# Kernel tuning notes

Measured on AMD Instinct MI355X. Metric: run time of the kernel, lower is better.

## Reference

```python
import jax, jax.numpy as jnp
import numpy as np

N = 50000
E = 800000
D_IN, D_HID, D_OUT = 256, 512, 256
LN_EPS = 1e-5


def setup_inputs() -> dict:
    key = jax.random.key(0)
    ks = jax.random.split(key, 8)
    return {
        "v": jax.random.normal(ks[0], (N, D_IN), dtype=jnp.float32),
        "edge_weight": jax.random.uniform(ks[1], (E,), dtype=jnp.float32),
        "epsilon": jnp.zeros((1, 1), dtype=jnp.float32),
        "w1": jax.random.normal(ks[2], (D_HID, D_IN), dtype=jnp.float32) * (1.0 / np.sqrt(D_IN)),
        "b1": jnp.zeros((D_HID,), dtype=jnp.float32),
        "g1": jnp.ones((D_HID,), dtype=jnp.float32),
        "beta1": jnp.zeros((D_HID,), dtype=jnp.float32),
        "w2": jax.random.normal(ks[3], (D_OUT, D_HID), dtype=jnp.float32) * (1.0 / np.sqrt(D_HID)),
        "b2": jnp.zeros((D_OUT,), dtype=jnp.float32),
        "g2": jnp.ones((D_OUT,), dtype=jnp.float32),
        "beta2": jnp.zeros((D_OUT,), dtype=jnp.float32),
        "src": jax.random.randint(ks[4], (E,), 0, N, dtype=jnp.int32),
        "dst": jax.random.randint(ks[5], (E,), 0, N, dtype=jnp.int32),
    }


def _layer_norm(x, g, b):
    mu = jnp.mean(x, axis=-1, keepdims=True)
    var = jnp.mean(jnp.square(x - mu), axis=-1, keepdims=True)
    return (x - mu) * jax.lax.rsqrt(var + LN_EPS) * g + b


def reference(v, edge_weight, epsilon, w1, b1, g1, beta1, w2, b2, g2, beta2, src, dst):
    # sparse adjacency aggregation: agg[dst] += w * v[src]   (torch.sparse.mm(a, v))
    msgs = v[src] * edge_weight[:, None]            # [E, D_IN]
    agg = jax.ops.segment_sum(msgs, dst, num_segments=v.shape[0])  # [N, D_IN]
    h = agg + epsilon * v                            # epsilon residual
    # MLP: Linear -> LayerNorm -> ReLU  (x2)
    h = jax.nn.relu(_layer_norm(h @ w1.T + b1, g1, beta1))
    h = jax.nn.relu(_layer_norm(h @ w2.T + b2, g2, beta2))
    return h
```

## Files before the change

kernel.cpp:

```cpp
#include <hip/hip_runtime.h>

#define D_IN 256
#define D_HID 512
#define D_OUT 256
#define LN_EPS 1e-5f
#define SCAN_B 512

typedef __attribute__((ext_vector_type(8))) short bf16x8;
typedef __attribute__((ext_vector_type(4))) float f32x4;

__device__ __forceinline__ ushort f2bf(float x) {
    union { float f; unsigned u; } c; c.f = x;
    unsigned r = c.u + 0x7FFFu + ((c.u >> 16) & 1u);
    return (ushort)(r >> 16);
}
__device__ __forceinline__ float bf2f(unsigned b) {
    union { unsigned u; float f; } c; c.u = b << 16;
    return c.f;
}

__global__ void prep_kernel(const float* __restrict__ v, const float* __restrict__ w1,
                            const float* __restrict__ w2, ushort* __restrict__ vb,
                            ushort* __restrict__ w1p, ushort* __restrict__ w2p,
                            int* __restrict__ cnt, int n4v, int nzero,
                            int bv, int bw) {
    int b = blockIdx.x, t = threadIdx.x;
    if (b < bv) {
        int i = b * 256 + t;
        if (i < n4v) {
            float4 x = ((const float4*)v)[i];
            ((ushort4*)vb)[i] = make_ushort4(f2bf(x.x), f2bf(x.y), f2bf(x.z), f2bf(x.w));
        }
    } else if (b < bv + bw) {
        int j = (b - bv) * 256 + t;
        if (j < 32768) {
            int f = j * 4;
            int row = f >> 8, col = f & 255;
            float4 x = ((const float4*)w1)[j];
            int rb = row >> 4, fr = row & 15;
            int kb32 = col >> 5, q = (col & 31) >> 3, e = col & 7;
            int chunk = (kb32 * 32 + rb) * 64 + q * 16 + fr;
            *(ushort4*)(w1p + chunk * 8 + e) =
                make_ushort4(f2bf(x.x), f2bf(x.y), f2bf(x.z), f2bf(x.w));
        } else {
            int k = j - 32768;
            int f = k * 4;
            int row = f >> 9, col = f & 511;
            float4 x = ((const float4*)w2)[k];
            int rb = row >> 4, fr = row & 15;
            int kb32 = col >> 5, q = (col & 31) >> 3, e = col & 7;
            int chunk = (kb32 * 16 + rb) * 64 + q * 16 + fr;
            *(ushort4*)(w2p + chunk * 8 + e) =
                make_ushort4(f2bf(x.x), f2bf(x.y), f2bf(x.z), f2bf(x.w));
        }
    } else {
        int i = (b - bv - bw) * 256 + t;
        if (i < nzero) cnt[i] = 0;
    }
}

__global__ void hist_kernel(const int* __restrict__ dst, int* __restrict__ cnt, int E) {
    int e = blockIdx.x * 256 + threadIdx.x;
    if (e < E) atomicAdd(&cnt[dst[e]], 1);
}

__global__ __launch_bounds__(SCAN_B) void scan1_kernel(const int* __restrict__ cnt,
                                                       int* __restrict__ offs,
                                                       int* __restrict__ bsum, int n) {
    __shared__ int s[SCAN_B];
    int i = blockIdx.x * SCAN_B + threadIdx.x;
    int x = (i < n) ? cnt[i] : 0;
    s[threadIdx.x] = x;
    __syncthreads();
    for (int o = 1; o < SCAN_B; o <<= 1) {
        int t = (threadIdx.x >= (unsigned)o) ? s[threadIdx.x - o] : 0;
        __syncthreads();
        s[threadIdx.x] += t;
        __syncthreads();
    }
    if (i < n) offs[i] = s[threadIdx.x] - x;
    if (threadIdx.x == SCAN_B - 1) bsum[blockIdx.x] = s[threadIdx.x];
}

__global__ __launch_bounds__(SCAN_B) void scan3_kernel(int* __restrict__ offs,
                                                       int* __restrict__ cursor,
                                                       const int* __restrict__ bsum,
                                                       int n, int E, int nb) {
    __shared__ int s[SCAN_B];
    int t = threadIdx.x;
    s[t] = (t < nb && t < (int)blockIdx.x) ? bsum[t] : 0;
    __syncthreads();
    for (int o = SCAN_B / 2; o > 0; o >>= 1) {
        if (t < o) s[t] += s[t + o];
        __syncthreads();
    }
    int base = s[0];
    int i = blockIdx.x * SCAN_B + t;
    if (i < n) {
        int v0 = offs[i] + base;
        offs[i] = v0;
        cursor[i] = v0;
    }
    if (i == 0) offs[n] = E;
}

__global__ void fill_kernel(const int* __restrict__ src, const int* __restrict__ dst,
                            const float* __restrict__ ew, int* __restrict__ cursor,
                            int2* __restrict__ perm, int E) {
    int e = blockIdx.x * 256 + threadIdx.x;
    if (e >= E) return;
    int p = atomicAdd(&cursor[dst[e]], 1);
    perm[p] = make_int2(src[e], __float_as_int(ew[e]));
}

__global__ __launch_bounds__(256) void aggregate_kernel(
    const ushort* __restrict__ vb, const float* __restrict__ eps_p,
    const int* __restrict__ offs, const int2* __restrict__ perm,
    ushort* __restrict__ aggb, int N) {
    int node = blockIdx.x * 4 + (threadIdx.x >> 6);
    if (node >= N) return;
    int lane = threadIdx.x & 63;
    int beg = offs[node], end = offs[node + 1];
    float a0 = 0.f, a1 = 0.f, a2 = 0.f, a3 = 0.f;
    float c0 = 0.f, c1 = 0.f, c2 = 0.f, c3 = 0.f;

    int i = beg;
    for (; i + 8 <= end; i += 8) {
        int2 p0 = perm[i + 0], p1 = perm[i + 1], p2 = perm[i + 2], p3 = perm[i + 3];
        int2 p4 = perm[i + 4], p5 = perm[i + 5], p6 = perm[i + 6], p7 = perm[i + 7];
        float w0 = __int_as_float(p0.y), w1 = __int_as_float(p1.y);
        float w2 = __int_as_float(p2.y), w3 = __int_as_float(p3.y);
        float w4 = __int_as_float(p4.y), w5 = __int_as_float(p5.y);
        float w6 = __int_as_float(p6.y), w7 = __int_as_float(p7.y);
        ushort4 r0 = ((const ushort4*)(vb + (size_t)p0.x * D_IN))[lane];
        ushort4 r1 = ((const ushort4*)(vb + (size_t)p1.x * D_IN))[lane];
        ushort4 r2 = ((const ushort4*)(vb + (size_t)p2.x * D_IN))[lane];
        ushort4 r3 = ((const ushort4*)(vb + (size_t)p3.x * D_IN))[lane];
        ushort4 r4 = ((const ushort4*)(vb + (size_t)p4.x * D_IN))[lane];
        ushort4 r5 = ((const ushort4*)(vb + (size_t)p5.x * D_IN))[lane];
        ushort4 r6 = ((const ushort4*)(vb + (size_t)p6.x * D_IN))[lane];
        ushort4 r7 = ((const ushort4*)(vb + (size_t)p7.x * D_IN))[lane];
        a0 += w0 * bf2f(r0.x) + w1 * bf2f(r1.x) + w2 * bf2f(r2.x) + w3 * bf2f(r3.x);
        a1 += w0 * bf2f(r0.y) + w1 * bf2f(r1.y) + w2 * bf2f(r2.y) + w3 * bf2f(r3.y);
        a2 += w0 * bf2f(r0.z) + w1 * bf2f(r1.z) + w2 * bf2f(r2.z) + w3 * bf2f(r3.z);
        a3 += w0 * bf2f(r0.w) + w1 * bf2f(r1.w) + w2 * bf2f(r2.w) + w3 * bf2f(r3.w);
        c0 += w4 * bf2f(r4.x) + w5 * bf2f(r5.x) + w6 * bf2f(r6.x) + w7 * bf2f(r7.x);
        c1 += w4 * bf2f(r4.y) + w5 * bf2f(r5.y) + w6 * bf2f(r6.y) + w7 * bf2f(r7.y);
        c2 += w4 * bf2f(r4.z) + w5 * bf2f(r5.z) + w6 * bf2f(r6.z) + w7 * bf2f(r7.z);
        c3 += w4 * bf2f(r4.w) + w5 * bf2f(r5.w) + w6 * bf2f(r6.w) + w7 * bf2f(r7.w);
    }
    for (; i + 4 <= end; i += 4) {
        int2 p0 = perm[i + 0], p1 = perm[i + 1], p2 = perm[i + 2], p3 = perm[i + 3];
        float w0 = __int_as_float(p0.y), w1 = __int_as_float(p1.y);
        float w2 = __int_as_float(p2.y), w3 = __int_as_float(p3.y);
        ushort4 r0 = ((const ushort4*)(vb + (size_t)p0.x * D_IN))[lane];
        ushort4 r1 = ((const ushort4*)(vb + (size_t)p1.x * D_IN))[lane];
        ushort4 r2 = ((const ushort4*)(vb + (size_t)p2.x * D_IN))[lane];
        ushort4 r3 = ((const ushort4*)(vb + (size_t)p3.x * D_IN))[lane];
        a0 += w0 * bf2f(r0.x) + w1 * bf2f(r1.x) + w2 * bf2f(r2.x) + w3 * bf2f(r3.x);
        a1 += w0 * bf2f(r0.y) + w1 * bf2f(r1.y) + w2 * bf2f(r2.y) + w3 * bf2f(r3.y);
        a2 += w0 * bf2f(r0.z) + w1 * bf2f(r1.z) + w2 * bf2f(r2.z) + w3 * bf2f(r3.z);
        a3 += w0 * bf2f(r0.w) + w1 * bf2f(r1.w) + w2 * bf2f(r2.w) + w3 * bf2f(r3.w);
    }
    for (; i < end; ++i) {
        int2 p = perm[i];
        float w = __int_as_float(p.y);
        ushort4 r = ((const ushort4*)(vb + (size_t)p.x * D_IN))[lane];
        a0 += w * bf2f(r.x); a1 += w * bf2f(r.y);
        a2 += w * bf2f(r.z); a3 += w * bf2f(r.w);
    }
    a0 += c0; a1 += c1; a2 += c2; a3 += c3;
    float eps = eps_p[0];
    ushort4 m = ((const ushort4*)(vb + (size_t)node * D_IN))[lane];
    a0 += eps * bf2f(m.x); a1 += eps * bf2f(m.y);
    a2 += eps * bf2f(m.z); a3 += eps * bf2f(m.w);
    ((ushort4*)(aggb + (size_t)node * D_IN))[lane] =
        make_ushort4(f2bf(a0), f2bf(a1), f2bf(a2), f2bf(a3));
}

#define HS_IDX(row, col) ((row) * 512 + ((col) ^ (((row) & 7) << 3)))
#define AT_IDX(row, col) ((row) * 256 + ((col) ^ (((row) & 7) << 3)))

__global__ __launch_bounds__(256, 2) void mlp_kernel(
    const ushort* __restrict__ A, const ushort* __restrict__ w1p,
    const ushort* __restrict__ w2p,
    const float* __restrict__ b1, const float* __restrict__ g1, const float* __restrict__ be1,
    const float* __restrict__ b2, const float* __restrict__ g2, const float* __restrict__ be2,
    float* __restrict__ out, int N) {
    __shared__ ushort hs[32768];
    __shared__ float redf[640];

    int t = threadIdx.x;
    int w = t >> 6, lane = t & 63;
    int row0 = blockIdx.x * 64;
    int fr = lane & 15, q = lane >> 4, kb = q * 8;

    #pragma unroll
    for (int j = 0; j < 8; ++j) {
        int p = (w * 8 + j) * 64 + lane;
        int row = p >> 5, cbs = p & 31;
        int colblk = cbs ^ (row & 7);
        int ar = row0 + row; if (ar > N - 1) ar = N - 1;
        const ushort* gp = A + (size_t)ar * D_IN + colblk * 8;
        __builtin_amdgcn_global_load_lds(
            (const __attribute__((address_space(1))) void*)gp,
            (__attribute__((address_space(3))) void*)(&hs[(w * 8 + j) * 512]),
            16, 0, 0);
    }

    bf16x8 bfb[2][8];
    #pragma unroll
    for (int c = 0; c < 8; ++c)
        bfb[0][c] = *(const bf16x8*)(w1p + (size_t)((0 * 32 + w * 8 + c) * 64 + lane) * 8);

    __syncthreads();

    f32x4 acc[4][8];
    #pragma unroll
    for (int m = 0; m < 4; ++m)
        #pragma unroll
        for (int c = 0; c < 8; ++c) {
            f32x4 z = {0.f, 0.f, 0.f, 0.f};
            acc[m][c] = z;
        }

    #pragma unroll
    for (int ks = 0; ks < 8; ++ks) {
        const int cur = ks & 1, nxt = cur ^ 1;
        if (ks < 7) {
            #pragma unroll
            for (int c = 0; c < 8; ++c)
                bfb[nxt][c] = *(const bf16x8*)(w1p +
                    (size_t)(((ks + 1) * 32 + w * 8 + c) * 64 + lane) * 8);
        }
        bf16x8 af[4];
        #pragma unroll
        for (int m = 0; m < 4; ++m)
            af[m] = *(const bf16x8*)&hs[AT_IDX(m * 16 + fr, ks * 32 + kb)];
        #pragma unroll
        for (int m = 0; m < 4; ++m)
            #pragma unroll
            for (int c = 0; c < 8; ++c)
                acc[m][c] = __builtin_amdgcn_mfma_f32_16x16x32_bf16(af[m], bfb[cur][c], acc[m][c], 0, 0, 0);
    }

    {
        float bi[8], gg[8], bb[8];
        #pragma unroll
        for (int c = 0; c < 8; ++c) {
            int col = w * 128 + c * 16 + fr;
            bi[c] = b1[col]; gg[c] = g1[col]; bb[c] = be1[col];
        }
        #pragma unroll
        for (int m = 0; m < 4; ++m) {
            #pragma unroll
            for (int r = 0; r < 4; ++r) {
                float s = 0.f, sq = 0.f;
                #pragma unroll
                for (int c = 0; c < 8; ++c) {
                    float x = acc[m][c][r] + bi[c];
                    acc[m][c][r] = x;
                    s += x; sq += x * x;
                }
                #pragma unroll
                for (int o = 1; o < 16; o <<= 1) {
                    s  += __shfl_xor(s, o, 64);
                    sq += __shfl_xor(sq, o, 64);
                }
                if (fr == 0) {
                    int row = m * 16 + q * 4 + r;
                    redf[row * 4 + w]       = s;
                    redf[256 + row * 4 + w] = sq;
                }
            }
        }
        __syncthreads();
        if (t < 64) {
            float s  = redf[t * 4 + 0] + redf[t * 4 + 1] + redf[t * 4 + 2] + redf[t * 4 + 3];
            float sq = redf[256 + t * 4 + 0] + redf[256 + t * 4 + 1] +
                       redf[256 + t * 4 + 2] + redf[256 + t * 4 + 3];
            float mu = s / (float)D_HID;
            float var = sq / (float)D_HID - mu * mu;
            redf[512 + t] = mu;
            redf[576 + t] = rsqrtf(var + LN_EPS);
        }
        __syncthreads();
        #pragma unroll
        for (int m = 0; m < 4; ++m) {
            #pragma unroll
            for (int r = 0; r < 4; ++r) {
                int row = m * 16 + q * 4 + r;
                float mu = redf[512 + row], rs = redf[576 + row];
                #pragma unroll
                for (int c = 0; c < 8; ++c) {
                    int col = w * 128 + c * 16 + fr;
                    float y = (acc[m][c][r] - mu) * rs * gg[c] + bb[c];
                    hs[HS_IDX(row, col)] = f2bf(fmaxf(y, 0.f));
                }
            }
        }
    }

    bf16x8 bf2b[2][4][2];
    #pragma unroll
    for (int c = 0; c < 4; ++c)
        #pragma unroll
        for (int h = 0; h < 2; ++h)
            bf2b[0][c][h] = *(const bf16x8*)(w2p +
                (size_t)(((0 + h) * 16 + w * 4 + c) * 64 + lane) * 8);

    __syncthreads();

    f32x4 acc2[4][4];
    #pragma unroll
    for (int m = 0; m < 4; ++m)
        #pragma unroll
        for (int c = 0; c < 4; ++c) {
            f32x4 z = {0.f, 0.f, 0.f, 0.f};
            acc2[m][c] = z;
        }

    #pragma unroll
    for (int s = 0; s < 8; ++s) {
        const int cur = s & 1, nxt = cur ^ 1;
        if (s < 7) {
            #pragma unroll
            for (int c = 0; c < 4; ++c)
                #pragma unroll
                for (int h = 0; h < 2; ++h)
                    bf2b[nxt][c][h] = *(const bf16x8*)(w2p +
                        (size_t)(((2 * (s + 1) + h) * 16 + w * 4 + c) * 64 + lane) * 8);
        }
        bf16x8 af2[4][2];
        #pragma unroll
        for (int m = 0; m < 4; ++m)
            #pragma unroll
            for (int h = 0; h < 2; ++h)
                af2[m][h] = *(const bf16x8*)&hs[HS_IDX(m * 16 + fr, s * 64 + h * 32 + kb)];
        #pragma unroll
        for (int m = 0; m < 4; ++m)
            #pragma unroll
            for (int c = 0; c < 4; ++c)
                #pragma unroll
                for (int h = 0; h < 2; ++h)
                    acc2[m][c] = __builtin_amdgcn_mfma_f32_16x16x32_bf16(af2[m][h], bf2b[cur][c][h], acc2[m][c], 0, 0, 0);
    }

    {
        float bi[4], gg[4], bb[4];
        #pragma unroll
        for (int c = 0; c < 4; ++c) {
            int col = w * 64 + c * 16 + fr;
            bi[c] = b2[col]; gg[c] = g2[col]; bb[c] = be2[col];
        }
        #pragma unroll
        for (int m = 0; m < 4; ++m) {
            #pragma unroll
            for (int r = 0; r < 4; ++r) {
                float s = 0.f, sq = 0.f;
                #pragma unroll
                for (int c = 0; c < 4; ++c) {
                    float x = acc2[m][c][r] + bi[c];
                    acc2[m][c][r] = x;
                    s += x; sq += x * x;
                }
                #pragma unroll
                for (int o = 1; o < 16; o <<= 1) {
                    s  += __shfl_xor(s, o, 64);
                    sq += __shfl_xor(sq, o, 64);
                }
                if (fr == 0) {
                    int row = m * 16 + q * 4 + r;
                    redf[row * 4 + w]       = s;
                    redf[256 + row * 4 + w] = sq;
                }
            }
        }
        __syncthreads();
        if (t < 64) {
            float s  = redf[t * 4 + 0] + redf[t * 4 + 1] + redf[t * 4 + 2] + redf[t * 4 + 3];
            float sq = redf[256 + t * 4 + 0] + redf[256 + t * 4 + 1] +
                       redf[256 + t * 4 + 2] + redf[256 + t * 4 + 3];
            float mu = s / (float)D_OUT;
            float var = sq / (float)D_OUT - mu * mu;
            redf[512 + t] = mu;
            redf[576 + t] = rsqrtf(var + LN_EPS);
        }
        __syncthreads();
        #pragma unroll
        for (int m = 0; m < 4; ++m) {
            #pragma unroll
            for (int r = 0; r < 4; ++r) {
                int row = m * 16 + q * 4 + r;
                int grow = row0 + row;
                if (grow >= N) continue;
                float mu = redf[512 + row], rs = redf[576 + row];
                #pragma unroll
                for (int c = 0; c < 4; ++c) {
                    int col = w * 64 + c * 16 + fr;
                    float y = (acc2[m][c][r] - mu) * rs * gg[c] + bb[c];
                    out[(size_t)grow * D_OUT + col] = fmaxf(y, 0.f);
                }
            }
        }
    }
}

extern "C" void kernel_launch(void* const* d_in, const int* in_sizes, int n_in,
                              void* d_out, int out_size, void* d_ws, size_t ws_size,
                              hipStream_t stream) {
    const float* v     = (const float*)d_in[0];
    const float* ew    = (const float*)d_in[1];
    const float* eps   = (const float*)d_in[2];
    const float* w1    = (const float*)d_in[3];
    const float* b1    = (const float*)d_in[4];
    const float* g1    = (const float*)d_in[5];
    const float* beta1 = (const float*)d_in[6];
    const float* w2    = (const float*)d_in[7];
    const float* b2    = (const float*)d_in[8];
    const float* g2    = (const float*)d_in[9];
    const float* beta2 = (const float*)d_in[10];
    const int*   src   = (const int*)d_in[11];
    const int*   dst   = (const int*)d_in[12];

    int N = in_sizes[0] / D_IN;
    int E = in_sizes[1];

    float* out = (float*)d_out;

    char* ws = (char*)d_ws;
    size_t off = 0;
    ushort* vb   = (ushort*)(ws + off); off += (size_t)N * D_IN * 2;
    ushort* aggb = (ushort*)(ws + off); off += (size_t)N * D_IN * 2;
    ushort* w1p  = (ushort*)(ws + off); off += (size_t)D_HID * D_IN * 2;
    ushort* w2p  = (ushort*)(ws + off); off += (size_t)D_OUT * D_HID * 2;
    int* offs     = (int*)(ws + off); off += (size_t)(N + 256) * 4;
    int* cursor   = (int*)(ws + off); off += (size_t)(N + 256) * 4;
    int* bsum     = (int*)(ws + off); off += 1024;
    int2* perm    = (int2*)(ws + off); off += (size_t)E * 8;

    int nb = (N + SCAN_B - 1) / SCAN_B;
    int n4v = N * (D_IN / 4);
    int bv = (n4v + 255) / 256;
    int bw = 256;
    int bz = (N + 255) / 256;

    prep_kernel<<<bv + bw + bz, 256, 0, stream>>>(v, w1, w2, vb, w1p, w2p,
                                                  cursor, n4v, N, bv, bw);

    hist_kernel<<<(E + 255) / 256, 256, 0, stream>>>(dst, cursor, E);
    scan1_kernel<<<nb, SCAN_B, 0, stream>>>(cursor, offs, bsum, N);
    scan3_kernel<<<nb, SCAN_B, 0, stream>>>(offs, cursor, bsum, N, E, nb);
    fill_kernel<<<(E + 255) / 256, 256, 0, stream>>>(src, dst, ew, cursor, perm, E);

    aggregate_kernel<<<(N + 3) / 4, 256, 0, stream>>>(vb, eps, offs, perm, aggb, N);

    int mblocks = (N + 63) / 64;
    mlp_kernel<<<mblocks, 256, 0, stream>>>(aggb, w1p, w2p,
                                            b1, g1, beta1, b2, g2, beta2, out, N);
}
```

Measured before the change: 322.6 us.

## Fuse aggregation into MLP kernel and build CSR with atomic ranks

Moves the gather-aggregation into the MLP kernel so each block aggregates its 64 rows straight into shared memory, which removes the aggb intermediate write/read and one kernel launch. The CSR build now records each edge's atomic rank during the histogram (merged into prep_kernel), so fill computes positions without a second atomic pass. Zeroing moves to hipMemsetAsync. The risk is that the MLP kernel now does the latency-bound gather with only 4 waves per block and 2 blocks per CU, so the aggregation may get less parallelism than the separate kernel had. It also adds an extra rank array write and read.

```diff
diff --git a/kernel.cpp b/kernel.cpp
--- a/kernel.cpp
+++ b/kernel.cpp
@@ -22,7 +22,8 @@
 __global__ void prep_kernel(const float* __restrict__ v, const float* __restrict__ w1,
                             const float* __restrict__ w2, ushort* __restrict__ vb,
                             ushort* __restrict__ w1p, ushort* __restrict__ w2p,
-                            int* __restrict__ cnt, int n4v, int nzero,
+                            const int* __restrict__ dst, int* __restrict__ rank,
+                            int* __restrict__ cnt, int n4v, int E,
                             int bv, int bw) {
     int b = blockIdx.x, t = threadIdx.x;
     if (b < bv) {
@@ -54,14 +55,9 @@
                 make_ushort4(f2bf(x.x), f2bf(x.y), f2bf(x.z), f2bf(x.w));
         }
     } else {
-        int i = (b - bv - bw) * 256 + t;
-        if (i < nzero) cnt[i] = 0;
-    }
-}
-
-__global__ void hist_kernel(const int* __restrict__ dst, int* __restrict__ cnt, int E) {
-    int e = blockIdx.x * 256 + threadIdx.x;
-    if (e < E) atomicAdd(&cnt[dst[e]], 1);
+        int e = (b - bv - bw) * 256 + t;
+        if (e < E) rank[e] = atomicAdd(&cnt[dst[e]], 1);
+    }
 }
 
 __global__ __launch_bounds__(SCAN_B) void scan1_kernel(const int* __restrict__ cnt,
@@ -83,7 +79,6 @@
 }
 
 __global__ __launch_bounds__(SCAN_B) void scan3_kernel(int* __restrict__ offs,
-                                                       int* __restrict__ cursor,
                                                        const int* __restrict__ bsum,
                                                        int n, int E, int nb) {
     __shared__ int s[SCAN_B];
@@ -96,94 +91,27 @@
     }
     int base = s[0];
     int i = blockIdx.x * SCAN_B + t;
-    if (i < n) {
-        int v0 = offs[i] + base;
-        offs[i] = v0;
-        cursor[i] = v0;
-    }
+    if (i < n) offs[i] += base;
     if (i == 0) offs[n] = E;
 }
 
 __global__ void fill_kernel(const int* __restrict__ src, const int* __restrict__ dst,
-                            const float* __restrict__ ew, int* __restrict__ cursor,
+                            const float* __restrict__ ew, const int* __restrict__ rank,
+                            const int* __restrict__ offs,
                             int2* __restrict__ perm, int E) {
     int e = blockIdx.x * 256 + threadIdx.x;
     if (e >= E) return;
-    int p = atomicAdd(&cursor[dst[e]], 1);
+    int p = offs[dst[e]] + rank[e];
     perm[p] = make_int2(src[e], __float_as_int(ew[e]));
 }
 
-__global__ __launch_bounds__(256) void aggregate_kernel(
+#define HS_IDX(row, col) ((row) * 512 + ((col) ^ (((row) & 7) << 3)))
+#define AT_IDX(row, col) ((row) * 256 + ((col) ^ (((row) & 7) << 3)))
+
+__global__ __launch_bounds__(256, 2) void mlp_kernel(
     const ushort* __restrict__ vb, const float* __restrict__ eps_p,
     const int* __restrict__ offs, const int2* __restrict__ perm,
-    ushort* __restrict__ aggb, int N) {
-    int node = blockIdx.x * 4 + (threadIdx.x >> 6);
-    if (node >= N) return;
-    int lane = threadIdx.x & 63;
-    int beg = offs[node], end = offs[node + 1];
-    float a0 = 0.f, a1 = 0.f, a2 = 0.f, a3 = 0.f;
-    float c0 = 0.f, c1 = 0.f, c2 = 0.f, c3 = 0.f;
-
-    int i = beg;
-    for (; i + 8 <= end; i += 8) {
-        int2 p0 = perm[i + 0], p1 = perm[i + 1], p2 = perm[i + 2], p3 = perm[i + 3];
-        int2 p4 = perm[i + 4], p5 = perm[i + 5], p6 = perm[i + 6], p7 = perm[i + 7];
-        float w0 = __int_as_float(p0.y), w1 = __int_as_float(p1.y);
-        float w2 = __int_as_float(p2.y), w3 = __int_as_float(p3.y);
-        float w4 = __int_as_float(p4.y), w5 = __int_as_float(p5.y);
-        float w6 = __int_as_float(p6.y), w7 = __int_as_float(p7.y);
-        ushort4 r0 = ((const ushort4*)(vb + (size_t)p0.x * D_IN))[lane];
-        ushort4 r1 = ((const ushort4*)(vb + (size_t)p1.x * D_IN))[lane];
-        ushort4 r2 = ((const ushort4*)(vb + (size_t)p2.x * D_IN))[lane];
-        ushort4 r3 = ((const ushort4*)(vb + (size_t)p3.x * D_IN))[lane];
-        ushort4 r4 = ((const ushort4*)(vb + (size_t)p4.x * D_IN))[lane];
-        ushort4 r5 = ((const ushort4*)(vb + (size_t)p5.x * D_IN))[lane];
-        ushort4 r6 = ((const ushort4*)(vb + (size_t)p6.x * D_IN))[lane];
-        ushort4 r7 = ((const ushort4*)(vb + (size_t)p7.x * D_IN))[lane];
-        a0 += w0 * bf2f(r0.x) + w1 * bf2f(r1.x) + w2 * bf2f(r2.x) + w3 * bf2f(r3.x);
-        a1 += w0 * bf2f(r0.y) + w1 * bf2f(r1.y) + w2 * bf2f(r2.y) + w3 * bf2f(r3.y);
-        a2 += w0 * bf2f(r0.z) + w1 * bf2f(r1.z) + w2 * bf2f(r2.z) + w3 * bf2f(r3.z);
-        a3 += w0 * bf2f(r0.w) + w1 * bf2f(r1.w) + w2 * bf2f(r2.w) + w3 * bf2f(r3.w);
-        c0 += w4 * bf2f(r4.x) + w5 * bf2f(r5.x) + w6 * bf2f(r6.x) + w7 * bf2f(r7.x);
-        c1 += w4 * bf2f(r4.y) + w5 * bf2f(r5.y) + w6 * bf2f(r6.y) + w7 * bf2f(r7.y);
-        c2 += w4 * bf2f(r4.z) + w5 * bf2f(r5.z) + w6 * bf2f(r6.z) + w7 * bf2f(r7.z);
-        c3 += w4 * bf2f(r4.w) + w5 * bf2f(r5.w) + w6 * bf2f(r6.w) + w7 * bf2f(r7.w);
-    }
-    for (; i + 4 <= end; i += 4) {
-        int2 p0 = perm[i + 0], p1 = perm[i + 1], p2 = perm[i + 2], p3 = perm[i + 3];
-        float w0 = __int_as_float(p0.y), w1 = __int_as_float(p1.y);
-        float w2 = __int_as_float(p2.y), w3 = __int_as_float(p3.y);
-        ushort4 r0 = ((const ushort4*)(vb + (size_t)p0.x * D_IN))[lane];
-        ushort4 r1 = ((const ushort4*)(vb + (size_t)p1.x * D_IN))[lane];
-        ushort4 r2 = ((const ushort4*)(vb + (size_t)p2.x * D_IN))[lane];
-        ushort4 r3 = ((const ushort4*)(vb + (size_t)p3.x * D_IN))[lane];
-        a0 += w0 * bf2f(r0.x) + w1 * bf2f(r1.x) + w2 * bf2f(r2.x) + w3 * bf2f(r3.x);
-        a1 += w0 * bf2f(r0.y) + w1 * bf2f(r1.y) + w2 * bf2f(r2.y) + w3 * bf2f(r3.y);
-        a2 += w0 * bf2f(r0.z) + w1 * bf2f(r1.z) + w2 * bf2f(r2.z) + w3 * bf2f(r3.z);
-        a3 += w0 * bf2f(r0.w) + w1 * bf2f(r1.w) + w2 * bf2f(r2.w) + w3 * bf2f(r3.w);
-    }
-    for (; i < end; ++i) {
-        int2 p = perm[i];
-        float w = __int_as_float(p.y);
-        ushort4 r = ((const ushort4*)(vb + (size_t)p.x * D_IN))[lane];
-        a0 += w * bf2f(r.x); a1 += w * bf2f(r.y);
-        a2 += w * bf2f(r.z); a3 += w * bf2f(r.w);
-    }
-    a0 += c0; a1 += c1; a2 += c2; a3 += c3;
-    float eps = eps_p[0];
-    ushort4 m = ((const ushort4*)(vb + (size_t)node * D_IN))[lane];
-    a0 += eps * bf2f(m.x); a1 += eps * bf2f(m.y);
-    a2 += eps * bf2f(m.z); a3 += eps * bf2f(m.w);
-    ((ushort4*)(aggb + (size_t)node * D_IN))[lane] =
-        make_ushort4(f2bf(a0), f2bf(a1), f2bf(a2), f2bf(a3));
-}
-
-#define HS_IDX(row, col) ((row) * 512 + ((col) ^ (((row) & 7) << 3)))
-#define AT_IDX(row, col) ((row) * 256 + ((col) ^ (((row) & 7) << 3)))
-
-__global__ __launch_bounds__(256, 2) void mlp_kernel(
-    const ushort* __restrict__ A, const ushort* __restrict__ w1p,
-    const ushort* __restrict__ w2p,
+    const ushort* __restrict__ w1p, const ushort* __restrict__ w2p,
     const float* __restrict__ b1, const float* __restrict__ g1, const float* __restrict__ be1,
     const float* __restrict__ b2, const float* __restrict__ g2, const float* __restrict__ be2,
     float* __restrict__ out, int N) {
@@ -195,23 +123,74 @@
     int row0 = blockIdx.x * 64;
     int fr = lane & 15, q = lane >> 4, kb = q * 8;
 
-    #pragma unroll
-    for (int j = 0; j < 8; ++j) {
-        int p = (w * 8 + j) * 64 + lane;
-        int row = p >> 5, cbs = p & 31;
-        int colblk = cbs ^ (row & 7);
-        int ar = row0 + row; if (ar > N - 1) ar = N - 1;
-        const ushort* gp = A + (size_t)ar * D_IN + colblk * 8;
-        __builtin_amdgcn_global_load_lds(
-            (const __attribute__((address_space(1))) void*)gp,
-            (__attribute__((address_space(3))) void*)(&hs[(w * 8 + j) * 512]),
-            16, 0, 0);
+    {
+        const float eps = eps_p[0];
+        for (int i = 0; i < 16; ++i) {
+            int r = w * 16 + i;
+            int node = row0 + r;
+            if (node > N - 1) node = N - 1;
+            int beg = offs[node], end = offs[node + 1];
+            float a0 = 0.f, a1 = 0.f, a2 = 0.f, a3 = 0.f;
+            float c0 = 0.f, c1 = 0.f, c2 = 0.f, c3 = 0.f;
+
+            int e = beg;
+            for (; e + 8 <= end; e += 8) {
+                int2 p0 = perm[e + 0], p1 = perm[e + 1], p2 = perm[e + 2], p3 = perm[e + 3];
+                int2 p4 = perm[e + 4], p5 = perm[e + 5], p6 = perm[e + 6], p7 = perm[e + 7];
+                float w0 = __int_as_float(p0.y), w1 = __int_as_float(p1.y);
+                float w2 = __int_as_float(p2.y), w3 = __int_as_float(p3.y);
+                float w4 = __int_as_float(p4.y), w5 = __int_as_float(p5.y);
+                float w6 = __int_as_float(p6.y), w7 = __int_as_float(p7.y);
+                ushort4 r0 = ((const ushort4*)(vb + (size_t)p0.x * D_IN))[lane];
+                ushort4 r1 = ((const ushort4*)(vb + (size_t)p1.x * D_IN))[lane];
+                ushort4 r2 = ((const ushort4*)(vb + (size_t)p2.x * D_IN))[lane];
+                ushort4 r3 = ((const ushort4*)(vb + (size_t)p3.x * D_IN))[lane];
+                ushort4 r4 = ((const ushort4*)(vb + (size_t)p4.x * D_IN))[lane];
+                ushort4 r5 = ((const ushort4*)(vb + (size_t)p5.x * D_IN))[lane];
+                ushort4 r6 = ((const ushort4*)(vb + (size_t)p6.x * D_IN))[lane];
+                ushort4 r7 = ((const ushort4*)(vb + (size_t)p7.x * D_IN))[lane];
+                a0 += w0 * bf2f(r0.x) + w1 * bf2f(r1.x) + w2 * bf2f(r2.x) + w3 * bf2f(r3.x);
+                a1 += w0 * bf2f(r0.y) + w1 * bf2f(r1.y) + w2 * bf2f(r2.y) + w3 * bf2f(r3.y);
+                a2 += w0 * bf2f(r0.z) + w1 * bf2f(r1.z) + w2 * bf2f(r2.z) + w3 * bf2f(r3.z);
+                a3 += w0 * bf2f(r0.w) + w1 * bf2f(r1.w) + w2 * bf2f(r2.w) + w3 * bf2f(r3.w);
+                c0 += w4 * bf2f(r4.x) + w5 * bf2f(r5.x) + w6 * bf2f(r6.x) + w7 * bf2f(r7.x);
+                c1 += w4 * bf2f(r4.y) + w5 * bf2f(r5.y) + w6 * bf2f(r6.y) + w7 * bf2f(r7.y);
+                c2 += w4 * bf2f(r4.z) + w5 * bf2f(r5.z) + w6 * bf2f(r6.z) + w7 * bf2f(r7.z);
+                c3 += w4 * bf2f(r4.w) + w5 * bf2f(r5.w) + w6 * bf2f(r6.w) + w7 * bf2f(r7.w);
+            }
+            for (; e + 4 <= end; e += 4) {
+                int2 p0 = perm[e + 0], p1 = perm[e + 1], p2 = perm[e + 2], p3 = perm[e + 3];
+                float w0 = __int_as_float(p0.y), w1 = __int_as_float(p1.y);
+                float w2 = __int_as_float(p2.y), w3 = __int_as_float(p3.y);
+                ushort4 r0 = ((const ushort4*)(vb + (size_t)p0.x * D_IN))[lane];
+                ushort4 r1 = ((const ushort4*)(vb + (size_t)p1.x * D_IN))[lane];
+                ushort4 r2 = ((const ushort4*)(vb + (size_t)p2.x * D_IN))[lane];
+                ushort4 r3 = ((const ushort4*)(vb + (size_t)p3.x * D_IN))[lane];
+                a0 += w0 * bf2f(r0.x) + w1 * bf2f(r1.x) + w2 * bf2f(r2.x) + w3 * bf2f(r3.x);
+                a1 += w0 * bf2f(r0.y) + w1 * bf2f(r1.y) + w2 * bf2f(r2.y) + w3 * bf2f(r3.y);
+                a2 += w0 * bf2f(r0.z) + w1 * bf2f(r1.z) + w2 * bf2f(r2.z) + w3 * bf2f(r3.z);
+                a3 += w0 * bf2f(r0.w) + w1 * bf2f(r1.w) + w2 * bf2f(r2.w) + w3 * bf2f(r3.w);
+            }
+            for (; e < end; ++e) {
+                int2 p = perm[e];
+                float we = __int_as_float(p.y);
+                ushort4 rr = ((const ushort4*)(vb + (size_t)p.x * D_IN))[lane];
+                a0 += we * bf2f(rr.x); a1 += we * bf2f(rr.y);
+                a2 += we * bf2f(rr.z); a3 += we * bf2f(rr.w);
+            }
+            a0 += c0; a1 += c1; a2 += c2; a3 += c3;
+            ushort4 mv = ((const ushort4*)(vb + (size_t)node * D_IN))[lane];
+            a0 += eps * bf2f(mv.x); a1 += eps * bf2f(mv.y);
+            a2 += eps * bf2f(mv.z); a3 += eps * bf2f(mv.w);
+            *(ushort4*)&hs[r * 256 + ((lane * 4) ^ ((r & 7) << 3))] =
+                make_ushort4(f2bf(a0), f2bf(a1), f2bf(a2), f2bf(a3));
+        }
     }
 
     bf16x8 bfb[2][8];
     #pragma unroll
     for (int c = 0; c < 8; ++c)
-        bfb[0][c] = *(const bf16x8*)(w1p + (size_t)((0 * 32 + w * 8 + c) * 64 + lane) * 8);
+        bfb[0][c] = *(const bf16x8*)(w1p + (size_t)((w * 8 + c) * 64 + lane) * 8);
 
     __syncthreads();
 
@@ -431,31 +410,31 @@
     char* ws = (char*)d_ws;
     size_t off = 0;
     ushort* vb   = (ushort*)(ws + off); off += (size_t)N * D_IN * 2;
-    ushort* aggb = (ushort*)(ws + off); off += (size_t)N * D_IN * 2;
     ushort* w1p  = (ushort*)(ws + off); off += (size_t)D_HID * D_IN * 2;
     ushort* w2p  = (ushort*)(ws + off); off += (size_t)D_OUT * D_HID * 2;
     int* offs     = (int*)(ws + off); off += (size_t)(N + 256) * 4;
-    int* cursor   = (int*)(ws + off); off += (size_t)(N + 256) * 4;
+    int* cnt      = (int*)(ws + off); off += (size_t)(N + 256) * 4;
     int* bsum     = (int*)(ws + off); off += 1024;
+    int* rank     = (int*)(ws + off); off += (size_t)E * 4;
     int2* perm    = (int2*)(ws + off); off += (size_t)E * 8;
 
     int nb = (N + SCAN_B - 1) / SCAN_B;
     int n4v = N * (D_IN / 4);
     int bv = (n4v + 255) / 256;
     int bw = 256;
-    int bz = (N + 255) / 256;
-
-    prep_kernel<<<bv + bw + bz, 256, 0, stream>>>(v, w1, w2, vb, w1p, w2p,
-                                                  cursor, n4v, N, bv, bw);
-
-    hist_kernel<<<(E + 255) / 256, 256, 0, stream>>>(dst, cursor, E);
-    scan1_kernel<<<nb, SCAN_B, 0, stream>>>(cursor, offs, bsum, N);
-    scan3_kernel<<<nb, SCAN_B, 0, stream>>>(offs, cursor, bsum, N, E, nb);
-    fill_kernel<<<(E + 255) / 256, 256, 0, stream>>>(src, dst, ew, cursor, perm, E);
-
-    aggregate_kernel<<<(N + 3) / 4, 256, 0, stream>>>(vb, eps, offs, perm, aggb, N);
+    int be = (E + 255) / 256;
+
+    hipMemsetAsync(cnt, 0, (size_t)N * 4, stream);
+
+    prep_kernel<<<bv + bw + be, 256, 0, stream>>>(v, w1, w2, vb, w1p, w2p,
+                                                  dst, rank, cnt, n4v, E, bv, bw);
+
+    scan1_kernel<<<nb, SCAN_B, 0, stream>>>(cnt, offs, bsum, N);
+    scan3_kernel<<<nb, SCAN_B, 0, stream>>>(offs, bsum, N, E, nb);
+
+    fill_kernel<<<be, 256, 0, stream>>>(src, dst, ew, rank, offs, perm, E);
 
     int mblocks = (N + 63) / 64;
-    mlp_kernel<<<mblocks, 256, 0, stream>>>(aggb, w1p, w2p,
+    mlp_kernel<<<mblocks, 256, 0, stream>>>(vb, eps, offs, perm, w1p, w2p,
                                             b1, g1, beta1, b2, g2, beta2, out, N);
 }
```

Result: slower. 345.3 us (+7.0%).
